# Performance work log

Hardware: AMD Instinct MI355X
Metric: run time of the kernel (lower is better)

## Reference

```python
import jax, jax.numpy as jnp
import numpy as np

N_NODES = 50000
N_EDGES = 800000
N_GRAPHS = 128
IN_DIM, H1, H2, OUT_DIM = 256, 128, 64, 10


def setup_inputs() -> dict:
    key = jax.random.key(0)
    ks = jax.random.split(key, 8)
    x = jax.random.normal(ks[0], (N_NODES, IN_DIM), dtype=jnp.float32)
    edge_index = jax.random.randint(ks[1], (2, N_EDGES), 0, N_NODES, dtype=jnp.int64 if jax.config.jax_enable_x64 else jnp.int32)
    batch = jnp.sort(jax.random.randint(ks[2], (N_NODES,), 0, N_GRAPHS))
    s1 = 1.0 / np.sqrt(IN_DIM)
    s2 = 1.0 / np.sqrt(H1)
    s3 = 1.0 / np.sqrt(H2)
    W1 = jax.random.uniform(ks[3], (IN_DIM, H1), jnp.float32, -s1, s1)
    b1 = jnp.zeros((H1,), jnp.float32)
    W2 = jax.random.uniform(ks[4], (H1, H2), jnp.float32, -s2, s2)
    b2 = jnp.zeros((H2,), jnp.float32)
    Wfc = jax.random.uniform(ks[5], (H2, OUT_DIM), jnp.float32, -s3, s3)
    bfc = jax.random.uniform(ks[6], (OUT_DIM,), jnp.float32, -s3, s3)
    return {"x": x, "edge_index": edge_index, "batch": batch,
            "W1": W1, "b1": b1, "W2": W2, "b2": b2, "Wfc": Wfc, "bfc": bfc}


def _gcn_norm(edge_index, n_nodes):
    # PyG gcn_norm with add_self_loops=True: D^{-1/2} (A+I) D^{-1/2}
    self_loops = jnp.arange(n_nodes, dtype=edge_index.dtype)
    row = jnp.concatenate([edge_index[0], self_loops])
    col = jnp.concatenate([edge_index[1], self_loops])
    deg = jax.ops.segment_sum(jnp.ones_like(col, dtype=jnp.float32), col,
                              num_segments=n_nodes)
    dis = jnp.where(deg > 0, 1.0 / jnp.sqrt(deg), 0.0)
    norm = dis[row] * dis[col]  # [E + N]
    return row, col, norm


def _gcn_layer(x, W, b, row, col, norm, n_nodes):
    h = x @ W                          # [N, out]
    msg = h[row] * norm[:, None]       # gather + scale: [E+N, out]
    agg = jax.ops.segment_sum(msg, col, num_segments=n_nodes)
    return jax.nn.relu(agg + b)


def reference(x, edge_index, batch, W1, b1, W2, b2, Wfc, bfc):
    n = x.shape[0]
    row, col, norm = _gcn_norm(edge_index, n)
    h = _gcn_layer(x, W1, b1, row, col, norm, n)
    h = _gcn_layer(h, W2, b2, row, col, norm, n)
    # global max pool over graphs
    g = jax.ops.segment_max(h, batch, num_segments=N_GRAPHS)  # [G, H2]
    # dropout is identity at inference
    return g @ Wfc + bfc
```

## Files before the change

kernel.cpp:

```cpp
#include <hip/hip_runtime.h>
#include <math.h>


typedef __attribute__((ext_vector_type(8))) short bfrag;
typedef __attribute__((ext_vector_type(4))) float ffrag;

__device__ inline void bf16split(float f, short& hi, short& lo) {
    unsigned u = __float_as_uint(f);
    unsigned r = u + 0x7fffu + ((u >> 16) & 1u);
    unsigned short h = (unsigned short)(r >> 16);
    float hf = __uint_as_float(((unsigned)h) << 16);
    float lf = f - hf;
    unsigned ul = __float_as_uint(lf);
    unsigned rl = ul + 0x7fffu + ((ul >> 16) & 1u);
    hi = (short)h;
    lo = (short)(rl >> 16);
}

__device__ inline unsigned short f2bf(float f) {
    unsigned u = __float_as_uint(f);
    unsigned r = u + 0x7fffu + ((u >> 16) & 1u);
    return (unsigned short)(r >> 16);
}

__global__ __launch_bounds__(256) void k_zero(int* __restrict__ cnt, int* __restrict__ pool,
                                              int n1, int n2) {
    int i = blockIdx.x * 256 + threadIdx.x;
    if (i < n1) cnt[i] = 0;
    if (i < n2) pool[i] = 0;
}

__global__ __launch_bounds__(256) void k_count(const int* __restrict__ ei, int* __restrict__ cnt,
                                               int E) {
    int e = blockIdx.x * 256 + threadIdx.x;
    if (e < E) atomicAdd(&cnt[ei[E + e]], 1);
}

__global__ __launch_bounds__(256) void k_dis(const int* __restrict__ cnt, float* __restrict__ dis,
                                             int N) {
    int v = blockIdx.x * 256 + threadIdx.x;
    if (v < N) dis[v] = 1.0f / sqrtf((float)(cnt[v] + 1));
}

__global__ __launch_bounds__(1024) void k_scan_block(const int* __restrict__ cnt,
                                                     int* __restrict__ rowptr,
                                                     int* __restrict__ bsum, int N) {
    __shared__ int lds[1024];
    int t = threadIdx.x;
    int i = blockIdx.x * 1024 + t;
    int val = (i < N) ? cnt[i] : 0;
    lds[t] = val;
    __syncthreads();
    for (int off = 1; off < 1024; off <<= 1) {
        int u = (t >= off) ? lds[t - off] : 0;
        __syncthreads();
        lds[t] += u;
        __syncthreads();
    }
    if (i < N) rowptr[i] = lds[t] - val;
    if (t == 1023) bsum[blockIdx.x] = lds[1023];
}

__global__ __launch_bounds__(1024) void k_scan_tot(const int* __restrict__ bsum,
                                                   int* __restrict__ bsum2, int nb) {
    __shared__ int lds[1024];
    int t = threadIdx.x;
    int val = (t < nb) ? bsum[t] : 0;
    lds[t] = val;
    __syncthreads();
    for (int off = 1; off < 1024; off <<= 1) {
        int u = (t >= off) ? lds[t - off] : 0;
        __syncthreads();
        lds[t] += u;
        __syncthreads();
    }
    if (t < nb) bsum2[t] = lds[t] - val;
}

__global__ __launch_bounds__(256) void k_scan_add(int* __restrict__ rowptr, int* __restrict__ cursor,
                                                  const int* __restrict__ bsum2, int N, int E) {
    int i = blockIdx.x * 256 + threadIdx.x;
    if (i < N) {
        int r = rowptr[i] + bsum2[i >> 10];
        rowptr[i] = r;
        cursor[i] = r;
    }
    if (i == 0) rowptr[N] = E;
}

__global__ __launch_bounds__(256) void k_fill(const int* __restrict__ ei,
                                              const float* __restrict__ dis,
                                              int* __restrict__ cursor,
                                              float2* __restrict__ csr, int E) {
    int e = blockIdx.x * 256 + threadIdx.x;
    if (e >= E) return;
    int r = ei[e];
    int c = ei[E + e];
    int p = atomicAdd(&cursor[c], 1);
    csr[p] = make_float2(__int_as_float(r), dis[r] * dis[c]);
}

__global__ __launch_bounds__(256) void k_wsplit(const float* __restrict__ W,
                                                short* __restrict__ wt_hi,
                                                short* __restrict__ wt_lo) {
    int i = blockIdx.x * 256 + threadIdx.x;
    if (i >= 256 * 128) return;
    int k = i >> 7, c = i & 127;
    short hi, lo;
    bf16split(W[i], hi, lo);
    wt_hi[c * 256 + k] = hi;
    wt_lo[c * 256 + k] = lo;
}

__global__ __launch_bounds__(256) void k_gemm1_mfma(const float* __restrict__ A,
                                                    const short* __restrict__ wt_hi,
                                                    const short* __restrict__ wt_lo,
                                                    unsigned short* __restrict__ C, int M) {
    constexpr int KD = 256;
    __shared__ short Ah[64][40];
    __shared__ short Al[64][40];

    const int t = threadIdx.x;
    const int lane = t & 63;
    const int wid = t >> 6;
    const int wr = wid >> 1;
    const int wc = wid & 1;
    const int row0 = blockIdx.x * 64;
    const int lrow = lane & 15;
    const int lkg = lane >> 4;

    ffrag acc[2][4];
#pragma unroll
    for (int mr = 0; mr < 2; mr++)
#pragma unroll
        for (int nr = 0; nr < 4; nr++)
#pragma unroll
            for (int q = 0; q < 4; q++) acc[mr][nr][q] = 0.f;

    for (int kc = 0; kc < KD; kc += 32) {
#pragma unroll
        for (int i = 0; i < 2; i++) {
            int s = t * 2 + i;
            int m = s >> 3;
            int kq = s & 7;
            int r = row0 + m;
            float4 v = make_float4(0.f, 0.f, 0.f, 0.f);
            if (r < M) v = *(const float4*)&A[(size_t)r * KD + kc + kq * 4];
            short4 sh, sl;
            bf16split(v.x, sh.x, sl.x);
            bf16split(v.y, sh.y, sl.y);
            bf16split(v.z, sh.z, sl.z);
            bf16split(v.w, sh.w, sl.w);
            *(short4*)&Ah[m][kq * 4] = sh;
            *(short4*)&Al[m][kq * 4] = sl;
        }
        __syncthreads();

        bfrag ahi[2], alo[2];
#pragma unroll
        for (int mr = 0; mr < 2; mr++) {
            int arow = wr * 32 + mr * 16 + lrow;
            ahi[mr] = *(const bfrag*)&Ah[arow][lkg * 8];
            alo[mr] = *(const bfrag*)&Al[arow][lkg * 8];
        }
#pragma unroll
        for (int nr = 0; nr < 4; nr++) {
            int col = wc * 64 + nr * 16 + lrow;
            const size_t boff = (size_t)col * 256 + kc + lkg * 8;
            bfrag bhi = *(const bfrag*)&wt_hi[boff];
            bfrag blo = *(const bfrag*)&wt_lo[boff];
#pragma unroll
            for (int mr = 0; mr < 2; mr++) {
                acc[mr][nr] = __builtin_amdgcn_mfma_f32_16x16x32_bf16(ahi[mr], bhi, acc[mr][nr], 0, 0, 0);
                acc[mr][nr] = __builtin_amdgcn_mfma_f32_16x16x32_bf16(ahi[mr], blo, acc[mr][nr], 0, 0, 0);
                acc[mr][nr] = __builtin_amdgcn_mfma_f32_16x16x32_bf16(alo[mr], bhi, acc[mr][nr], 0, 0, 0);
            }
        }
        __syncthreads();
    }

#pragma unroll
    for (int mr = 0; mr < 2; mr++)
#pragma unroll
        for (int nr = 0; nr < 4; nr++)
#pragma unroll
            for (int q = 0; q < 4; q++) {
                int rr = row0 + wr * 32 + mr * 16 + lkg * 4 + q;
                int cc = wc * 64 + nr * 16 + lrow;
                if (rr < M) C[(size_t)rr * 128 + cc] = f2bf(acc[mr][nr][q]);
            }
}

__global__ __launch_bounds__(256) void k_gemm2(const float* __restrict__ A,
                                               const float* __restrict__ W,
                                               unsigned short* __restrict__ C, int M) {
    constexpr int KDIM = 128, NOUT = 64, BM = 64, BK = 32;
    __shared__ float As[BK][BM + 4];
    __shared__ float Ws[BK][NOUT];

    const int t = threadIdx.x;
    const int tx = t & 15;
    const int ty = t >> 4;
    const int row0 = blockIdx.x * BM;

    float acc[4][4];
#pragma unroll
    for (int r = 0; r < 4; r++)
#pragma unroll
        for (int c = 0; c < 4; c++) acc[r][c] = 0.f;

    for (int kc = 0; kc < KDIM; kc += BK) {
#pragma unroll
        for (int i = 0; i < 2; i++) {
            int s = t * 2 + i;
            int m = s >> 3;
            int kq = s & 7;
            int r = row0 + m;
            float4 v = make_float4(0.f, 0.f, 0.f, 0.f);
            if (r < M) v = *(const float4*)&A[(size_t)r * KDIM + kc + kq * 4];
            As[kq * 4 + 0][m] = v.x;
            As[kq * 4 + 1][m] = v.y;
            As[kq * 4 + 2][m] = v.z;
            As[kq * 4 + 3][m] = v.w;
        }
#pragma unroll
        for (int i = 0; i < 2; i++) {
            int s = t + i * 256;
            int k = s / 16;
            int c4 = s % 16;
            *(float4*)&Ws[k][c4 * 4] = *(const float4*)&W[(size_t)(kc + k) * NOUT + c4 * 4];
        }
        __syncthreads();

#pragma unroll
        for (int k = 0; k < BK; k++) {
            float4 a = *(const float4*)&As[k][ty * 4];
            float4 w0 = *(const float4*)&Ws[k][tx * 4];
            const float* ap = (const float*)&a;
            const float* w0p = (const float*)&w0;
#pragma unroll
            for (int r = 0; r < 4; r++)
#pragma unroll
                for (int c = 0; c < 4; c++) acc[r][c] += ap[r] * w0p[c];
        }
        __syncthreads();
    }

#pragma unroll
    for (int r = 0; r < 4; r++) {
        int rr = row0 + ty * 4 + r;
        if (rr < M) {
            ushort4 o;
            o.x = f2bf(acc[r][0]);
            o.y = f2bf(acc[r][1]);
            o.z = f2bf(acc[r][2]);
            o.w = f2bf(acc[r][3]);
            *(ushort4*)&C[(size_t)rr * NOUT + tx * 4] = o;
        }
    }
}

__global__ __launch_bounds__(256) void k_agg1(const unsigned int* __restrict__ h1b,
                                              const int* __restrict__ rowptr,
                                              const float2* __restrict__ csr,
                                              const float* __restrict__ dis,
                                              const float* __restrict__ b,
                                              float* __restrict__ out, int N) {
    int wave = (blockIdx.x * 256 + threadIdx.x) >> 6;
    int lane = threadIdx.x & 63;
    if (wave >= N) return;
    const int v = wave;
    float d = dis[v];
    float ds2 = d * d;
    unsigned hv = h1b[(size_t)v * 64 + lane];
    float ax = ds2 * __uint_as_float(hv << 16);
    float ay = ds2 * __uint_as_float(hv & 0xffff0000u);
    int s0 = rowptr[v], s1 = rowptr[v + 1];
    for (int j = s0; j < s1; j += 8) {
        int   uu[8];
        float ww[8];
#pragma unroll
        for (int q = 0; q < 8; q++) {
            int jj = j + q;
            bool ok = jj < s1;
            float2 e = csr[ok ? jj : s0];
            uu[q] = ok ? __float_as_int(e.x) : 0;
            ww[q] = ok ? e.y : 0.f;
        }
        unsigned g[8];
#pragma unroll
        for (int q = 0; q < 8; q++) g[q] = h1b[(size_t)uu[q] * 64 + lane];
#pragma unroll
        for (int q = 0; q < 8; q++) {
            ax += ww[q] * __uint_as_float(g[q] << 16);
            ay += ww[q] * __uint_as_float(g[q] & 0xffff0000u);
        }
    }
    float2 bb = *(const float2*)&b[lane * 2];
    float2 o;
    o.x = fmaxf(ax + bb.x, 0.f);
    o.y = fmaxf(ay + bb.y, 0.f);
    *(float2*)&out[(size_t)v * 128 + lane * 2] = o;
}

__global__ __launch_bounds__(256) void k_agg2_pool(const unsigned short* __restrict__ h2b,
                                                   const int* __restrict__ rowptr,
                                                   const float2* __restrict__ csr,
                                                   const float* __restrict__ dis,
                                                   const float* __restrict__ b,
                                                   const int* __restrict__ batch,
                                                   float* __restrict__ pool, int N) {
    int wave = (blockIdx.x * 256 + threadIdx.x) >> 6;
    int lane = threadIdx.x & 63;
    if (wave >= N) return;
    const int v = wave;
    float d = dis[v];
    float ds2 = d * d;
    float acc = ds2 * __uint_as_float(((unsigned)h2b[(size_t)v * 64 + lane]) << 16);
    int s0 = rowptr[v], s1 = rowptr[v + 1];
    for (int j = s0; j < s1; j += 8) {
        int   uu[8];
        float ww[8];
#pragma unroll
        for (int q = 0; q < 8; q++) {
            int jj = j + q;
            bool ok = jj < s1;
            float2 e = csr[ok ? jj : s0];
            uu[q] = ok ? __float_as_int(e.x) : 0;
            ww[q] = ok ? e.y : 0.f;
        }
        unsigned short g[8];
#pragma unroll
        for (int q = 0; q < 8; q++) g[q] = h2b[(size_t)uu[q] * 64 + lane];
#pragma unroll
        for (int q = 0; q < 8; q++) acc += ww[q] * __uint_as_float(((unsigned)g[q]) << 16);
    }
    float val = fmaxf(acc + b[lane], 0.f);
    int g = batch[v];
    atomicMax((int*)&pool[(size_t)g * 64 + lane], __float_as_int(val));
}

__global__ __launch_bounds__(256) void k_fc(const float* __restrict__ pool,
                                            const float* __restrict__ Wfc,
                                            const float* __restrict__ bfc,
                                            float* __restrict__ out, int G) {
    int t = blockIdx.x * 256 + threadIdx.x;
    if (t >= G * 10) return;
    int g = t / 10, o = t % 10;
    float acc = bfc[o];
#pragma unroll
    for (int f = 0; f < 64; f++) acc += pool[g * 64 + f] * Wfc[f * 10 + o];
    out[t] = acc;
}

extern "C" void kernel_launch(void* const* d_in, const int* in_sizes, int n_in,
                              void* d_out, int out_size, void* d_ws, size_t ws_size,
                              hipStream_t stream) {
    const float* x   = (const float*)d_in[0];
    const int*   ei  = (const int*)d_in[1];
    const int*   bat = (const int*)d_in[2];
    const float* W1  = (const float*)d_in[3];
    const float* b1  = (const float*)d_in[4];
    const float* W2  = (const float*)d_in[5];
    const float* b2  = (const float*)d_in[6];
    const float* Wfc = (const float*)d_in[7];
    const float* bfc = (const float*)d_in[8];
    float* out = (float*)d_out;

    const int N = in_sizes[2];
    const int E = in_sizes[1] / 2;
    const int G = out_size / 10;

    char* ws = (char*)d_ws;
    size_t off = 0;
    auto alloc = [&](size_t bytes) -> char* {
        char* p = ws + off;
        off = (off + bytes + 255) & ~(size_t)255;
        return p;
    };
    int*    cnt    = (int*)alloc((size_t)N * 4);
    float*  dis    = (float*)alloc((size_t)N * 4);
    int*    rowptr = (int*)alloc((size_t)(N + 1) * 4);
    int*    cursor = (int*)alloc((size_t)N * 4);
    int*    bsum   = (int*)alloc(1024 * 4);
    int*    bsum2  = (int*)alloc(1024 * 4);
    float2* csr    = (float2*)alloc((size_t)E * 8);
    unsigned short* h1b = (unsigned short*)alloc((size_t)N * 128 * 2);
    float*  a1     = (float*)alloc((size_t)N * 128 * 4);
    unsigned short* h2b = (unsigned short*)alloc((size_t)N * 64 * 2);
    float*  pool   = (float*)alloc((size_t)G * 64 * 4);
    short*  wt_hi  = (short*)alloc(128 * 256 * 2);
    short*  wt_lo  = (short*)alloc(128 * 256 * 2);
    (void)ws_size; (void)n_in;

    const int nb = (N + 1023) / 1024;

    {
        int zmax = N > G * 64 ? N : G * 64;
        k_zero<<<(zmax + 255) / 256, 256, 0, stream>>>(cnt, (int*)pool, N, G * 64);
    }
    k_wsplit<<<128, 256, 0, stream>>>(W1, wt_hi, wt_lo);
    k_count<<<(E + 255) / 256, 256, 0, stream>>>(ei, cnt, E);
    k_dis<<<(N + 255) / 256, 256, 0, stream>>>(cnt, dis, N);
    k_scan_block<<<nb, 1024, 0, stream>>>(cnt, rowptr, bsum, N);
    k_scan_tot<<<1, 1024, 0, stream>>>(bsum, bsum2, nb);
    k_scan_add<<<(N + 255) / 256, 256, 0, stream>>>(rowptr, cursor, bsum2, N, E);
    k_fill<<<(E + 255) / 256, 256, 0, stream>>>(ei, dis, cursor, csr, E);

    k_gemm1_mfma<<<(N + 63) / 64, 256, 0, stream>>>(x, wt_hi, wt_lo, h1b, N);
    k_agg1<<<(N * 64 + 255) / 256, 256, 0, stream>>>((const unsigned int*)h1b, rowptr, csr,
                                                     dis, b1, a1, N);

    k_gemm2<<<(N + 63) / 64, 256, 0, stream>>>(a1, W2, h2b, N);
    k_agg2_pool<<<(N * 64 + 255) / 256, 256, 0, stream>>>(h2b, rowptr, csr, dis, b2, bat,
                                                          pool, N);

    k_fc<<<(G * 10 + 255) / 256, 256, 0, stream>>>(pool, Wfc, bfc, out, G);
}
```

Before: 367.0 us.

## Split each wave into two half-waves processing alternate edges with wider gathers

Each node's CSR segment is padded to an even length so edge entries can be read in pairs as float4. Each half of the wave takes one edge of the pair and gathers two or four bf16 features per lane using wider loads. The halves are summed with a cross-half shuffle before bias, ReLU and the store or atomic max. The intent is to halve the number of serial gather iterations per node and use wider memory transactions, at the cost of padding and a shuffle reduction. Segment ends now come from the count array rather than rowptr[v+1].

```diff
diff --git a/kernel.cpp b/kernel.cpp
--- a/kernel.cpp
+++ b/kernel.cpp
@@ -23,6 +23,9 @@
     return (unsigned short)(r >> 16);
 }
 
+__device__ inline float bfl(unsigned u) { return __uint_as_float(u << 16); }
+__device__ inline float bfh(unsigned u) { return __uint_as_float(u & 0xffff0000u); }
+
 __global__ __launch_bounds__(256) void k_zero(int* __restrict__ cnt, int* __restrict__ pool,
                                               int n1, int n2) {
     int i = blockIdx.x * 256 + threadIdx.x;
@@ -48,7 +51,7 @@
     __shared__ int lds[1024];
     int t = threadIdx.x;
     int i = blockIdx.x * 1024 + t;
-    int val = (i < N) ? cnt[i] : 0;
+    int val = (i < N) ? ((cnt[i] + 1) & ~1) : 0;
     lds[t] = val;
     __syncthreads();
     for (int off = 1; off < 1024; off <<= 1) {
@@ -78,14 +81,13 @@
 }
 
 __global__ __launch_bounds__(256) void k_scan_add(int* __restrict__ rowptr, int* __restrict__ cursor,
-                                                  const int* __restrict__ bsum2, int N, int E) {
+                                                  const int* __restrict__ bsum2, int N) {
     int i = blockIdx.x * 256 + threadIdx.x;
     if (i < N) {
         int r = rowptr[i] + bsum2[i >> 10];
         rowptr[i] = r;
         cursor[i] = r;
     }
-    if (i == 0) rowptr[N] = E;
 }
 
 __global__ __launch_bounds__(256) void k_fill(const int* __restrict__ ei,
@@ -260,9 +262,10 @@
     }
 }
 
-__global__ __launch_bounds__(256) void k_agg1(const unsigned int* __restrict__ h1b,
+__global__ __launch_bounds__(256) void k_agg1(const uint2* __restrict__ h,
                                               const int* __restrict__ rowptr,
-                                              const float2* __restrict__ csr,
+                                              const int* __restrict__ cnt,
+                                              const float4* __restrict__ csr2,
                                               const float* __restrict__ dis,
                                               const float* __restrict__ b,
                                               float* __restrict__ out, int N) {
@@ -270,42 +273,57 @@
     int lane = threadIdx.x & 63;
     if (wave >= N) return;
     const int v = wave;
+    const int half = lane >> 5;
+    const int hl = lane & 31;
     float d = dis[v];
-    float ds2 = d * d;
-    unsigned hv = h1b[(size_t)v * 64 + lane];
-    float ax = ds2 * __uint_as_float(hv << 16);
-    float ay = ds2 * __uint_as_float(hv & 0xffff0000u);
-    int s0 = rowptr[v], s1 = rowptr[v + 1];
+    float selfw = half ? 0.f : d * d;
+    uint2 sv = h[(size_t)v * 32 + hl];
+    float a0 = selfw * bfl(sv.x), a1 = selfw * bfh(sv.x);
+    float a2 = selfw * bfl(sv.y), a3 = selfw * bfh(sv.y);
+    int s0 = rowptr[v], s1 = s0 + cnt[v];
     for (int j = s0; j < s1; j += 8) {
-        int   uu[8];
-        float ww[8];
-#pragma unroll
-        for (int q = 0; q < 8; q++) {
-            int jj = j + q;
+        int   uu[4];
+        float ww[4];
+#pragma unroll
+        for (int q = 0; q < 4; q++) {
+            float4 ce = csr2[(j >> 1) + q];
+            int jj = j + 2 * q + half;
             bool ok = jj < s1;
-            float2 e = csr[ok ? jj : s0];
-            uu[q] = ok ? __float_as_int(e.x) : 0;
-            ww[q] = ok ? e.y : 0.f;
-        }
-        unsigned g[8];
-#pragma unroll
-        for (int q = 0; q < 8; q++) g[q] = h1b[(size_t)uu[q] * 64 + lane];
-#pragma unroll
-        for (int q = 0; q < 8; q++) {
-            ax += ww[q] * __uint_as_float(g[q] << 16);
-            ay += ww[q] * __uint_as_float(g[q] & 0xffff0000u);
-        }
-    }
-    float2 bb = *(const float2*)&b[lane * 2];
-    float2 o;
-    o.x = fmaxf(ax + bb.x, 0.f);
-    o.y = fmaxf(ay + bb.y, 0.f);
-    *(float2*)&out[(size_t)v * 128 + lane * 2] = o;
-}
-
-__global__ __launch_bounds__(256) void k_agg2_pool(const unsigned short* __restrict__ h2b,
+            float ux = half ? ce.z : ce.x;
+            float wx = half ? ce.w : ce.y;
+            uu[q] = ok ? __float_as_int(ux) : 0;
+            ww[q] = ok ? wx : 0.f;
+        }
+        uint2 g[4];
+#pragma unroll
+        for (int q = 0; q < 4; q++) g[q] = h[(size_t)uu[q] * 32 + hl];
+#pragma unroll
+        for (int q = 0; q < 4; q++) {
+            a0 += ww[q] * bfl(g[q].x);
+            a1 += ww[q] * bfh(g[q].x);
+            a2 += ww[q] * bfl(g[q].y);
+            a3 += ww[q] * bfh(g[q].y);
+        }
+    }
+    a0 += __shfl_xor(a0, 32);
+    a1 += __shfl_xor(a1, 32);
+    a2 += __shfl_xor(a2, 32);
+    a3 += __shfl_xor(a3, 32);
+    if (half == 0) {
+        float4 bb = *(const float4*)&b[hl * 4];
+        float4 o;
+        o.x = fmaxf(a0 + bb.x, 0.f);
+        o.y = fmaxf(a1 + bb.y, 0.f);
+        o.z = fmaxf(a2 + bb.z, 0.f);
+        o.w = fmaxf(a3 + bb.w, 0.f);
+        *(float4*)&out[(size_t)v * 128 + hl * 4] = o;
+    }
+}
+
+__global__ __launch_bounds__(256) void k_agg2_pool(const unsigned int* __restrict__ h,
                                                    const int* __restrict__ rowptr,
-                                                   const float2* __restrict__ csr,
+                                                   const int* __restrict__ cnt,
+                                                   const float4* __restrict__ csr2,
                                                    const float* __restrict__ dis,
                                                    const float* __restrict__ b,
                                                    const int* __restrict__ batch,
@@ -314,30 +332,45 @@
     int lane = threadIdx.x & 63;
     if (wave >= N) return;
     const int v = wave;
+    const int half = lane >> 5;
+    const int hl = lane & 31;
     float d = dis[v];
-    float ds2 = d * d;
-    float acc = ds2 * __uint_as_float(((unsigned)h2b[(size_t)v * 64 + lane]) << 16);
-    int s0 = rowptr[v], s1 = rowptr[v + 1];
+    float selfw = half ? 0.f : d * d;
+    unsigned sv = h[(size_t)v * 32 + hl];
+    float a0 = selfw * bfl(sv), a1 = selfw * bfh(sv);
+    int s0 = rowptr[v], s1 = s0 + cnt[v];
     for (int j = s0; j < s1; j += 8) {
-        int   uu[8];
-        float ww[8];
-#pragma unroll
-        for (int q = 0; q < 8; q++) {
-            int jj = j + q;
+        int   uu[4];
+        float ww[4];
+#pragma unroll
+        for (int q = 0; q < 4; q++) {
+            float4 ce = csr2[(j >> 1) + q];
+            int jj = j + 2 * q + half;
             bool ok = jj < s1;
-            float2 e = csr[ok ? jj : s0];
-            uu[q] = ok ? __float_as_int(e.x) : 0;
-            ww[q] = ok ? e.y : 0.f;
-        }
-        unsigned short g[8];
-#pragma unroll
-        for (int q = 0; q < 8; q++) g[q] = h2b[(size_t)uu[q] * 64 + lane];
-#pragma unroll
-        for (int q = 0; q < 8; q++) acc += ww[q] * __uint_as_float(((unsigned)g[q]) << 16);
-    }
-    float val = fmaxf(acc + b[lane], 0.f);
-    int g = batch[v];
-    atomicMax((int*)&pool[(size_t)g * 64 + lane], __float_as_int(val));
+            float ux = half ? ce.z : ce.x;
+            float wx = half ? ce.w : ce.y;
+            uu[q] = ok ? __float_as_int(ux) : 0;
+            ww[q] = ok ? wx : 0.f;
+        }
+        unsigned g[4];
+#pragma unroll
+        for (int q = 0; q < 4; q++) g[q] = h[(size_t)uu[q] * 32 + hl];
+#pragma unroll
+        for (int q = 0; q < 4; q++) {
+            a0 += ww[q] * bfl(g[q]);
+            a1 += ww[q] * bfh(g[q]);
+        }
+    }
+    a0 += __shfl_xor(a0, 32);
+    a1 += __shfl_xor(a1, 32);
+    if (half == 0) {
+        float2 bb = *(const float2*)&b[hl * 2];
+        float v0 = fmaxf(a0 + bb.x, 0.f);
+        float v1 = fmaxf(a1 + bb.y, 0.f);
+        int g = batch[v];
+        atomicMax((int*)&pool[(size_t)g * 64 + hl * 2], __float_as_int(v0));
+        atomicMax((int*)&pool[(size_t)g * 64 + hl * 2 + 1], __float_as_int(v1));
+    }
 }
 
 __global__ __launch_bounds__(256) void k_fc(const float* __restrict__ pool,
@@ -384,7 +417,7 @@
     int*    cursor = (int*)alloc((size_t)N * 4);
     int*    bsum   = (int*)alloc(1024 * 4);
     int*    bsum2  = (int*)alloc(1024 * 4);
-    float2* csr    = (float2*)alloc((size_t)E * 8);
+    float2* csr    = (float2*)alloc((size_t)(E + N + 8) * 8);
     unsigned short* h1b = (unsigned short*)alloc((size_t)N * 128 * 2);
     float*  a1     = (float*)alloc((size_t)N * 128 * 4);
     unsigned short* h2b = (unsigned short*)alloc((size_t)N * 64 * 2);
@@ -404,15 +437,16 @@
     k_dis<<<(N + 255) / 256, 256, 0, stream>>>(cnt, dis, N);
     k_scan_block<<<nb, 1024, 0, stream>>>(cnt, rowptr, bsum, N);
     k_scan_tot<<<1, 1024, 0, stream>>>(bsum, bsum2, nb);
-    k_scan_add<<<(N + 255) / 256, 256, 0, stream>>>(rowptr, cursor, bsum2, N, E);
+    k_scan_add<<<(N + 255) / 256, 256, 0, stream>>>(rowptr, cursor, bsum2, N);
     k_fill<<<(E + 255) / 256, 256, 0, stream>>>(ei, dis, cursor, csr, E);
 
     k_gemm1_mfma<<<(N + 63) / 64, 256, 0, stream>>>(x, wt_hi, wt_lo, h1b, N);
-    k_agg1<<<(N * 64 + 255) / 256, 256, 0, stream>>>((const unsigned int*)h1b, rowptr, csr,
-                                                     dis, b1, a1, N);
+    k_agg1<<<(N * 64 + 255) / 256, 256, 0, stream>>>((const uint2*)h1b, rowptr, cnt,
+                                                     (const float4*)csr, dis, b1, a1, N);
 
     k_gemm2<<<(N + 63) / 64, 256, 0, stream>>>(a1, W2, h2b, N);
-    k_agg2_pool<<<(N * 64 + 255) / 256, 256, 0, stream>>>(h2b, rowptr, csr, dis, b2, bat,
+    k_agg2_pool<<<(N * 64 + 255) / 256, 256, 0, stream>>>((const unsigned int*)h2b, rowptr, cnt,
+                                                          (const float4*)csr, dis, b2, bat,
                                                           pool, N);
 
     k_fc<<<(G * 10 + 255) / 256, 256, 0, stream>>>(pool, Wfc, bfc, out, G);
```

Result: slower. 375.2 us (+2.2%).

## Fuse layer-2 GEMM into layer-1 aggregation via wave shuffles

Applied to the files above, without the earlier changes.

Removes the separate layer-2 GEMM kernel and the fp32 intermediate a1 buffer. Each wave now finishes aggregating one node, then multiplies its 128-wide activation row by W2 using lane shuffles against a pre-paired W2 layout, and writes the bf16 h2 row directly. This cuts the write and re-read of the N×128 fp32 intermediate and one kernel launch. In exchange, each wave does 64 shuffle iterations of serial FMA work plus W2 reads from global/L2 memory instead of a shared-memory tiled GEMM.

```diff
diff --git a/kernel.cpp b/kernel.cpp
--- a/kernel.cpp
+++ b/kernel.cpp
@@ -22,6 +22,9 @@
     unsigned r = u + 0x7fffu + ((u >> 16) & 1u);
     return (unsigned short)(r >> 16);
 }
+
+__device__ inline float bfl(unsigned u) { return __uint_as_float(u << 16); }
+__device__ inline float bfh(unsigned u) { return __uint_as_float(u & 0xffff0000u); }
 
 __global__ __launch_bounds__(256) void k_zero(int* __restrict__ cnt, int* __restrict__ pool,
                                               int n1, int n2) {
@@ -110,6 +113,14 @@
     bf16split(W[i], hi, lo);
     wt_hi[c * 256 + k] = hi;
     wt_lo[c * 256 + k] = lo;
+}
+
+__global__ __launch_bounds__(256) void k_w2pair(const float* __restrict__ W2,
+                                                float2* __restrict__ w2p) {
+    int i = blockIdx.x * 256 + threadIdx.x;
+    if (i >= 64 * 64) return;
+    int kk = i >> 6, c = i & 63;
+    w2p[i] = make_float2(W2[(2 * kk) * 64 + c], W2[(2 * kk + 1) * 64 + c]);
 }
 
 __global__ __launch_bounds__(256) void k_gemm1_mfma(const float* __restrict__ A,
@@ -191,81 +202,13 @@
             }
 }
 
-__global__ __launch_bounds__(256) void k_gemm2(const float* __restrict__ A,
-                                               const float* __restrict__ W,
-                                               unsigned short* __restrict__ C, int M) {
-    constexpr int KDIM = 128, NOUT = 64, BM = 64, BK = 32;
-    __shared__ float As[BK][BM + 4];
-    __shared__ float Ws[BK][NOUT];
-
-    const int t = threadIdx.x;
-    const int tx = t & 15;
-    const int ty = t >> 4;
-    const int row0 = blockIdx.x * BM;
-
-    float acc[4][4];
-#pragma unroll
-    for (int r = 0; r < 4; r++)
-#pragma unroll
-        for (int c = 0; c < 4; c++) acc[r][c] = 0.f;
-
-    for (int kc = 0; kc < KDIM; kc += BK) {
-#pragma unroll
-        for (int i = 0; i < 2; i++) {
-            int s = t * 2 + i;
-            int m = s >> 3;
-            int kq = s & 7;
-            int r = row0 + m;
-            float4 v = make_float4(0.f, 0.f, 0.f, 0.f);
-            if (r < M) v = *(const float4*)&A[(size_t)r * KDIM + kc + kq * 4];
-            As[kq * 4 + 0][m] = v.x;
-            As[kq * 4 + 1][m] = v.y;
-            As[kq * 4 + 2][m] = v.z;
-            As[kq * 4 + 3][m] = v.w;
-        }
-#pragma unroll
-        for (int i = 0; i < 2; i++) {
-            int s = t + i * 256;
-            int k = s / 16;
-            int c4 = s % 16;
-            *(float4*)&Ws[k][c4 * 4] = *(const float4*)&W[(size_t)(kc + k) * NOUT + c4 * 4];
-        }
-        __syncthreads();
-
-#pragma unroll
-        for (int k = 0; k < BK; k++) {
-            float4 a = *(const float4*)&As[k][ty * 4];
-            float4 w0 = *(const float4*)&Ws[k][tx * 4];
-            const float* ap = (const float*)&a;
-            const float* w0p = (const float*)&w0;
-#pragma unroll
-            for (int r = 0; r < 4; r++)
-#pragma unroll
-                for (int c = 0; c < 4; c++) acc[r][c] += ap[r] * w0p[c];
-        }
-        __syncthreads();
-    }
-
-#pragma unroll
-    for (int r = 0; r < 4; r++) {
-        int rr = row0 + ty * 4 + r;
-        if (rr < M) {
-            ushort4 o;
-            o.x = f2bf(acc[r][0]);
-            o.y = f2bf(acc[r][1]);
-            o.z = f2bf(acc[r][2]);
-            o.w = f2bf(acc[r][3]);
-            *(ushort4*)&C[(size_t)rr * NOUT + tx * 4] = o;
-        }
-    }
-}
-
-__global__ __launch_bounds__(256) void k_agg1(const unsigned int* __restrict__ h1b,
-                                              const int* __restrict__ rowptr,
-                                              const float2* __restrict__ csr,
-                                              const float* __restrict__ dis,
-                                              const float* __restrict__ b,
-                                              float* __restrict__ out, int N) {
+__global__ __launch_bounds__(256) void k_agg1_g2(const unsigned int* __restrict__ h1b,
+                                                 const int* __restrict__ rowptr,
+                                                 const float2* __restrict__ csr,
+                                                 const float* __restrict__ dis,
+                                                 const float* __restrict__ b1,
+                                                 const float2* __restrict__ w2p,
+                                                 unsigned short* __restrict__ h2b, int N) {
     int wave = (blockIdx.x * 256 + threadIdx.x) >> 6;
     int lane = threadIdx.x & 63;
     if (wave >= N) return;
@@ -273,8 +216,8 @@
     float d = dis[v];
     float ds2 = d * d;
     unsigned hv = h1b[(size_t)v * 64 + lane];
-    float ax = ds2 * __uint_as_float(hv << 16);
-    float ay = ds2 * __uint_as_float(hv & 0xffff0000u);
+    float ax = ds2 * bfl(hv);
+    float ay = ds2 * bfh(hv);
     int s0 = rowptr[v], s1 = rowptr[v + 1];
     for (int j = s0; j < s1; j += 8) {
         int   uu[8];
@@ -292,15 +235,23 @@
         for (int q = 0; q < 8; q++) g[q] = h1b[(size_t)uu[q] * 64 + lane];
 #pragma unroll
         for (int q = 0; q < 8; q++) {
-            ax += ww[q] * __uint_as_float(g[q] << 16);
-            ay += ww[q] * __uint_as_float(g[q] & 0xffff0000u);
-        }
-    }
-    float2 bb = *(const float2*)&b[lane * 2];
-    float2 o;
-    o.x = fmaxf(ax + bb.x, 0.f);
-    o.y = fmaxf(ay + bb.y, 0.f);
-    *(float2*)&out[(size_t)v * 128 + lane * 2] = o;
+            ax += ww[q] * bfl(g[q]);
+            ay += ww[q] * bfh(g[q]);
+        }
+    }
+    float2 bb = *(const float2*)&b1[lane * 2];
+    float a0 = fmaxf(ax + bb.x, 0.f);
+    float a1v = fmaxf(ay + bb.y, 0.f);
+
+    float acc = 0.f;
+#pragma unroll 8
+    for (int kk = 0; kk < 64; kk++) {
+        float2 w = w2p[kk * 64 + lane];
+        float e0 = __shfl(a0, kk);
+        float e1 = __shfl(a1v, kk);
+        acc += e0 * w.x + e1 * w.y;
+    }
+    h2b[(size_t)v * 64 + lane] = f2bf(acc);
 }
 
 __global__ __launch_bounds__(256) void k_agg2_pool(const unsigned short* __restrict__ h2b,
@@ -386,11 +337,11 @@
     int*    bsum2  = (int*)alloc(1024 * 4);
     float2* csr    = (float2*)alloc((size_t)E * 8);
     unsigned short* h1b = (unsigned short*)alloc((size_t)N * 128 * 2);
-    float*  a1     = (float*)alloc((size_t)N * 128 * 4);
     unsigned short* h2b = (unsigned short*)alloc((size_t)N * 64 * 2);
     float*  pool   = (float*)alloc((size_t)G * 64 * 4);
     short*  wt_hi  = (short*)alloc(128 * 256 * 2);
     short*  wt_lo  = (short*)alloc(128 * 256 * 2);
+    float2* w2p    = (float2*)alloc(64 * 64 * 8);
     (void)ws_size; (void)n_in;
 
     const int nb = (N + 1023) / 1024;
@@ -400,6 +351,7 @@
         k_zero<<<(zmax + 255) / 256, 256, 0, stream>>>(cnt, (int*)pool, N, G * 64);
     }
     k_wsplit<<<128, 256, 0, stream>>>(W1, wt_hi, wt_lo);
+    k_w2pair<<<16, 256, 0, stream>>>(W2, w2p);
     k_count<<<(E + 255) / 256, 256, 0, stream>>>(ei, cnt, E);
     k_dis<<<(N + 255) / 256, 256, 0, stream>>>(cnt, dis, N);
     k_scan_block<<<nb, 1024, 0, stream>>>(cnt, rowptr, bsum, N);
@@ -408,10 +360,10 @@
     k_fill<<<(E + 255) / 256, 256, 0, stream>>>(ei, dis, cursor, csr, E);
 
     k_gemm1_mfma<<<(N + 63) / 64, 256, 0, stream>>>(x, wt_hi, wt_lo, h1b, N);
-    k_agg1<<<(N * 64 + 255) / 256, 256, 0, stream>>>((const unsigned int*)h1b, rowptr, csr,
-                                                     dis, b1, a1, N);
-
-    k_gemm2<<<(N + 63) / 64, 256, 0, stream>>>(a1, W2, h2b, N);
+
+    k_agg1_g2<<<(N * 64 + 255) / 256, 256, 0, stream>>>((const unsigned int*)h1b, rowptr, csr,
+                                                        dis, b1, w2p, h2b, N);
+
     k_agg2_pool<<<(N * 64 + 255) / 256, 256, 0, stream>>>(h2b, rowptr, csr, dis, b2, bat,
                                                           pool, N);
 
```

Result: slower. 424.8 us (+15.7%).

## Factor symmetric GCN normalization into GEMM epilogues and drop per-edge weights

Applied to the files above, without the earlier changes.

The D^-1/2 normalization is split so the source-side scale is applied in the GEMM epilogues and the destination-side scale after aggregation. The CSR therefore stores only int source indices instead of (index, weight) pairs, which halves edge-list traffic and removes a multiply per edge. Several small setup kernels are also merged: weight split with zeroing, dis with the block scan, and the serial block-sum prefix into the scan finalize. The catch is that bf16 rounding now happens after scaling, and a single thread runs a serial prefix loop in every block.

```diff
diff --git a/kernel.cpp b/kernel.cpp
--- a/kernel.cpp
+++ b/kernel.cpp
@@ -23,11 +23,24 @@
     return (unsigned short)(r >> 16);
 }
 
-__global__ __launch_bounds__(256) void k_zero(int* __restrict__ cnt, int* __restrict__ pool,
+__device__ inline float bfl(unsigned u) { return __uint_as_float(u << 16); }
+__device__ inline float bfh(unsigned u) { return __uint_as_float(u & 0xffff0000u); }
+
+__global__ __launch_bounds__(256) void k_prep(int* __restrict__ cnt, int* __restrict__ pool,
+                                              const float* __restrict__ W1,
+                                              short* __restrict__ wt_hi,
+                                              short* __restrict__ wt_lo,
                                               int n1, int n2) {
     int i = blockIdx.x * 256 + threadIdx.x;
     if (i < n1) cnt[i] = 0;
     if (i < n2) pool[i] = 0;
+    if (i < 256 * 128) {
+        int k = i >> 7, c = i & 127;
+        short hi, lo;
+        bf16split(W1[i], hi, lo);
+        wt_hi[c * 256 + k] = hi;
+        wt_lo[c * 256 + k] = lo;
+    }
 }
 
 __global__ __launch_bounds__(256) void k_count(const int* __restrict__ ei, int* __restrict__ cnt,
@@ -36,19 +49,15 @@
     if (e < E) atomicAdd(&cnt[ei[E + e]], 1);
 }
 
-__global__ __launch_bounds__(256) void k_dis(const int* __restrict__ cnt, float* __restrict__ dis,
-                                             int N) {
-    int v = blockIdx.x * 256 + threadIdx.x;
-    if (v < N) dis[v] = 1.0f / sqrtf((float)(cnt[v] + 1));
-}
-
-__global__ __launch_bounds__(1024) void k_scan_block(const int* __restrict__ cnt,
-                                                     int* __restrict__ rowptr,
-                                                     int* __restrict__ bsum, int N) {
+__global__ __launch_bounds__(1024) void k_scan_dis(const int* __restrict__ cnt,
+                                                   int* __restrict__ rowptr,
+                                                   int* __restrict__ bsum,
+                                                   float* __restrict__ dis, int N) {
     __shared__ int lds[1024];
     int t = threadIdx.x;
     int i = blockIdx.x * 1024 + t;
     int val = (i < N) ? cnt[i] : 0;
+    if (i < N) dis[i] = 1.0f / sqrtf((float)(val + 1));
     lds[t] = val;
     __syncthreads();
     for (int off = 1; off < 1024; off <<= 1) {
@@ -61,27 +70,20 @@
     if (t == 1023) bsum[blockIdx.x] = lds[1023];
 }
 
-__global__ __launch_bounds__(1024) void k_scan_tot(const int* __restrict__ bsum,
-                                                   int* __restrict__ bsum2, int nb) {
-    __shared__ int lds[1024];
+__global__ __launch_bounds__(256) void k_scan_fin(int* __restrict__ rowptr,
+                                                  int* __restrict__ cursor,
+                                                  const int* __restrict__ bsum,
+                                                  int nb, int N, int E) {
+    __shared__ int pre[128];
     int t = threadIdx.x;
-    int val = (t < nb) ? bsum[t] : 0;
-    lds[t] = val;
+    if (t == 0) {
+        int run = 0;
+        for (int q = 0; q < nb; q++) { pre[q] = run; run += bsum[q]; }
+    }
     __syncthreads();
-    for (int off = 1; off < 1024; off <<= 1) {
-        int u = (t >= off) ? lds[t - off] : 0;
-        __syncthreads();
-        lds[t] += u;
-        __syncthreads();
-    }
-    if (t < nb) bsum2[t] = lds[t] - val;
-}
-
-__global__ __launch_bounds__(256) void k_scan_add(int* __restrict__ rowptr, int* __restrict__ cursor,
-                                                  const int* __restrict__ bsum2, int N, int E) {
-    int i = blockIdx.x * 256 + threadIdx.x;
+    int i = blockIdx.x * 256 + t;
     if (i < N) {
-        int r = rowptr[i] + bsum2[i >> 10];
+        int r = rowptr[i] + pre[i >> 10];
         rowptr[i] = r;
         cursor[i] = r;
     }
@@ -89,32 +91,20 @@
 }
 
 __global__ __launch_bounds__(256) void k_fill(const int* __restrict__ ei,
-                                              const float* __restrict__ dis,
                                               int* __restrict__ cursor,
-                                              float2* __restrict__ csr, int E) {
+                                              int* __restrict__ csr_i, int E) {
     int e = blockIdx.x * 256 + threadIdx.x;
     if (e >= E) return;
     int r = ei[e];
     int c = ei[E + e];
     int p = atomicAdd(&cursor[c], 1);
-    csr[p] = make_float2(__int_as_float(r), dis[r] * dis[c]);
-}
-
-__global__ __launch_bounds__(256) void k_wsplit(const float* __restrict__ W,
-                                                short* __restrict__ wt_hi,
-                                                short* __restrict__ wt_lo) {
-    int i = blockIdx.x * 256 + threadIdx.x;
-    if (i >= 256 * 128) return;
-    int k = i >> 7, c = i & 127;
-    short hi, lo;
-    bf16split(W[i], hi, lo);
-    wt_hi[c * 256 + k] = hi;
-    wt_lo[c * 256 + k] = lo;
+    csr_i[p] = r;
 }
 
 __global__ __launch_bounds__(256) void k_gemm1_mfma(const float* __restrict__ A,
                                                     const short* __restrict__ wt_hi,
                                                     const short* __restrict__ wt_lo,
+                                                    const float* __restrict__ dis,
                                                     unsigned short* __restrict__ C, int M) {
     constexpr int KD = 256;
     __shared__ short Ah[64][40];
@@ -187,12 +177,13 @@
             for (int q = 0; q < 4; q++) {
                 int rr = row0 + wr * 32 + mr * 16 + lkg * 4 + q;
                 int cc = wc * 64 + nr * 16 + lrow;
-                if (rr < M) C[(size_t)rr * 128 + cc] = f2bf(acc[mr][nr][q]);
+                if (rr < M) C[(size_t)rr * 128 + cc] = f2bf(dis[rr] * acc[mr][nr][q]);
             }
 }
 
 __global__ __launch_bounds__(256) void k_gemm2(const float* __restrict__ A,
                                                const float* __restrict__ W,
+                                               const float* __restrict__ dis,
                                                unsigned short* __restrict__ C, int M) {
     constexpr int KDIM = 128, NOUT = 64, BM = 64, BK = 32;
     __shared__ float As[BK][BM + 4];
@@ -250,19 +241,20 @@
     for (int r = 0; r < 4; r++) {
         int rr = row0 + ty * 4 + r;
         if (rr < M) {
+            float dd = dis[rr];
             ushort4 o;
-            o.x = f2bf(acc[r][0]);
-            o.y = f2bf(acc[r][1]);
-            o.z = f2bf(acc[r][2]);
-            o.w = f2bf(acc[r][3]);
+            o.x = f2bf(dd * acc[r][0]);
+            o.y = f2bf(dd * acc[r][1]);
+            o.z = f2bf(dd * acc[r][2]);
+            o.w = f2bf(dd * acc[r][3]);
             *(ushort4*)&C[(size_t)rr * NOUT + tx * 4] = o;
         }
     }
 }
 
-__global__ __launch_bounds__(256) void k_agg1(const unsigned int* __restrict__ h1b,
+__global__ __launch_bounds__(256) void k_agg1(const unsigned int* __restrict__ hs1,
                                               const int* __restrict__ rowptr,
-                                              const float2* __restrict__ csr,
+                                              const int* __restrict__ csr_i,
                                               const float* __restrict__ dis,
                                               const float* __restrict__ b,
                                               float* __restrict__ out, int N) {
@@ -270,42 +262,37 @@
     int lane = threadIdx.x & 63;
     if (wave >= N) return;
     const int v = wave;
-    float d = dis[v];
-    float ds2 = d * d;
-    unsigned hv = h1b[(size_t)v * 64 + lane];
-    float ax = ds2 * __uint_as_float(hv << 16);
-    float ay = ds2 * __uint_as_float(hv & 0xffff0000u);
+    unsigned hv = hs1[(size_t)v * 64 + lane];
+    float ax = bfl(hv);
+    float ay = bfh(hv);
     int s0 = rowptr[v], s1 = rowptr[v + 1];
     for (int j = s0; j < s1; j += 8) {
-        int   uu[8];
-        float ww[8];
+        int uu[8];
 #pragma unroll
         for (int q = 0; q < 8; q++) {
             int jj = j + q;
-            bool ok = jj < s1;
-            float2 e = csr[ok ? jj : s0];
-            uu[q] = ok ? __float_as_int(e.x) : 0;
-            ww[q] = ok ? e.y : 0.f;
+            uu[q] = (jj < s1) ? csr_i[jj] : -1;
         }
         unsigned g[8];
 #pragma unroll
-        for (int q = 0; q < 8; q++) g[q] = h1b[(size_t)uu[q] * 64 + lane];
+        for (int q = 0; q < 8; q++) g[q] = (uu[q] >= 0) ? hs1[(size_t)uu[q] * 64 + lane] : 0u;
 #pragma unroll
         for (int q = 0; q < 8; q++) {
-            ax += ww[q] * __uint_as_float(g[q] << 16);
-            ay += ww[q] * __uint_as_float(g[q] & 0xffff0000u);
-        }
-    }
+            ax += bfl(g[q]);
+            ay += bfh(g[q]);
+        }
+    }
+    float d = dis[v];
     float2 bb = *(const float2*)&b[lane * 2];
     float2 o;
-    o.x = fmaxf(ax + bb.x, 0.f);
-    o.y = fmaxf(ay + bb.y, 0.f);
+    o.x = fmaxf(d * ax + bb.x, 0.f);
+    o.y = fmaxf(d * ay + bb.y, 0.f);
     *(float2*)&out[(size_t)v * 128 + lane * 2] = o;
 }
 
-__global__ __launch_bounds__(256) void k_agg2_pool(const unsigned short* __restrict__ h2b,
+__global__ __launch_bounds__(256) void k_agg2_pool(const unsigned short* __restrict__ hs2,
                                                    const int* __restrict__ rowptr,
-                                                   const float2* __restrict__ csr,
+                                                   const int* __restrict__ csr_i,
                                                    const float* __restrict__ dis,
                                                    const float* __restrict__ b,
                                                    const int* __restrict__ batch,
@@ -314,28 +301,23 @@
     int lane = threadIdx.x & 63;
     if (wave >= N) return;
     const int v = wave;
-    float d = dis[v];
-    float ds2 = d * d;
-    float acc = ds2 * __uint_as_float(((unsigned)h2b[(size_t)v * 64 + lane]) << 16);
+    float acc = __uint_as_float(((unsigned)hs2[(size_t)v * 64 + lane]) << 16);
     int s0 = rowptr[v], s1 = rowptr[v + 1];
     for (int j = s0; j < s1; j += 8) {
-        int   uu[8];
-        float ww[8];
+        int uu[8];
 #pragma unroll
         for (int q = 0; q < 8; q++) {
             int jj = j + q;
-            bool ok = jj < s1;
-            float2 e = csr[ok ? jj : s0];
-            uu[q] = ok ? __float_as_int(e.x) : 0;
-            ww[q] = ok ? e.y : 0.f;
+            uu[q] = (jj < s1) ? csr_i[jj] : -1;
         }
         unsigned short g[8];
 #pragma unroll
-        for (int q = 0; q < 8; q++) g[q] = h2b[(size_t)uu[q] * 64 + lane];
-#pragma unroll
-        for (int q = 0; q < 8; q++) acc += ww[q] * __uint_as_float(((unsigned)g[q]) << 16);
-    }
-    float val = fmaxf(acc + b[lane], 0.f);
+        for (int q = 0; q < 8; q++)
+            g[q] = (uu[q] >= 0) ? hs2[(size_t)uu[q] * 64 + lane] : (unsigned short)0;
+#pragma unroll
+        for (int q = 0; q < 8; q++) acc += __uint_as_float(((unsigned)g[q]) << 16);
+    }
+    float val = fmaxf(dis[v] * acc + b[lane], 0.f);
     int g = batch[v];
     atomicMax((int*)&pool[(size_t)g * 64 + lane], __float_as_int(val));
 }
@@ -383,36 +365,30 @@
     int*    rowptr = (int*)alloc((size_t)(N + 1) * 4);
     int*    cursor = (int*)alloc((size_t)N * 4);
     int*    bsum   = (int*)alloc(1024 * 4);
-    int*    bsum2  = (int*)alloc(1024 * 4);
-    float2* csr    = (float2*)alloc((size_t)E * 8);
-    unsigned short* h1b = (unsigned short*)alloc((size_t)N * 128 * 2);
+    int*    csr_i  = (int*)alloc((size_t)E * 4);
+    unsigned short* hs1 = (unsigned short*)alloc((size_t)N * 128 * 2);
     float*  a1     = (float*)alloc((size_t)N * 128 * 4);
-    unsigned short* h2b = (unsigned short*)alloc((size_t)N * 64 * 2);
+    unsigned short* hs2 = (unsigned short*)alloc((size_t)N * 64 * 2);
     float*  pool   = (float*)alloc((size_t)G * 64 * 4);
     short*  wt_hi  = (short*)alloc(128 * 256 * 2);
     short*  wt_lo  = (short*)alloc(128 * 256 * 2);
     (void)ws_size; (void)n_in;
 
     const int nb = (N + 1023) / 1024;
-
-    {
-        int zmax = N > G * 64 ? N : G * 64;
-        k_zero<<<(zmax + 255) / 256, 256, 0, stream>>>(cnt, (int*)pool, N, G * 64);
-    }
-    k_wsplit<<<128, 256, 0, stream>>>(W1, wt_hi, wt_lo);
+    const int nb256 = (N + 255) / 256;
+
+    k_prep<<<nb256, 256, 0, stream>>>(cnt, (int*)pool, W1, wt_hi, wt_lo, N, G * 64);
     k_count<<<(E + 255) / 256, 256, 0, stream>>>(ei, cnt, E);
-    k_dis<<<(N + 255) / 256, 256, 0, stream>>>(cnt, dis, N);
-    k_scan_block<<<nb, 1024, 0, stream>>>(cnt, rowptr, bsum, N);
-    k_scan_tot<<<1, 1024, 0, stream>>>(bsum, bsum2, nb);
-    k_scan_add<<<(N + 255) / 256, 256, 0, stream>>>(rowptr, cursor, bsum2, N, E);
-    k_fill<<<(E + 255) / 256, 256, 0, stream>>>(ei, dis, cursor, csr, E);
-
-    k_gemm1_mfma<<<(N + 63) / 64, 256, 0, stream>>>(x, wt_hi, wt_lo, h1b, N);
-    k_agg1<<<(N * 64 + 255) / 256, 256, 0, stream>>>((const unsigned int*)h1b, rowptr, csr,
+    k_scan_dis<<<nb, 1024, 0, stream>>>(cnt, rowptr, bsum, dis, N);
+    k_scan_fin<<<nb256, 256, 0, stream>>>(rowptr, cursor, bsum, nb, N, E);
+    k_fill<<<(E + 255) / 256, 256, 0, stream>>>(ei, cursor, csr_i, E);
+
+    k_gemm1_mfma<<<(N + 63) / 64, 256, 0, stream>>>(x, wt_hi, wt_lo, dis, hs1, N);
+    k_agg1<<<(N * 64 + 255) / 256, 256, 0, stream>>>((const unsigned int*)hs1, rowptr, csr_i,
                                                      dis, b1, a1, N);
 
-    k_gemm2<<<(N + 63) / 64, 256, 0, stream>>>(a1, W2, h2b, N);
-    k_agg2_pool<<<(N * 64 + 255) / 256, 256, 0, stream>>>(h2b, rowptr, csr, dis, b2, bat,
+    k_gemm2<<<(N + 63) / 64, 256, 0, stream>>>(a1, W2, dis, hs2, N);
+    k_agg2_pool<<<(N * 64 + 255) / 256, 256, 0, stream>>>(hs2, rowptr, csr_i, dis, b2, bat,
                                                           pool, N);
 
     k_fc<<<(G * 10 + 255) / 256, 256, 0, stream>>>(pool, Wfc, bfc, out, G);
```

After: 357.9 us. 1.03x faster.
